# Kernel tuning notes

Hardware: AMD Instinct MI355X
Metric: run time of the kernel (lower is better)

The kernel has to match this reference:

```python
import jax, jax.numpy as jnp
import numpy as np

HEAD_NUM = 16
HIDDEN = 1024
HEAD_DIM = HIDDEN // HEAD_NUM


def setup_inputs() -> dict:
    key = jax.random.key(0)
    ks = jax.random.split(key, 9)
    B, S, D = 1, 4096, HIDDEN
    scale = 1.0 / np.sqrt(D)
    inp = {
        "x": jax.random.normal(ks[0], (B, S, D), jnp.float32),
        "wq": jax.random.normal(ks[1], (D, D), jnp.float32) * scale,
        "bq": jnp.zeros((D,), jnp.float32),
        "wk": jax.random.normal(ks[2], (D, D), jnp.float32) * scale,
        "bk": jnp.zeros((D,), jnp.float32),
        "wv": jax.random.normal(ks[3], (D, D), jnp.float32) * scale,
        "bv": jnp.zeros((D,), jnp.float32),
        "wo": jax.random.normal(ks[4], (D, D), jnp.float32) * scale,
        "bo": jnp.zeros((D,), jnp.float32),
    }
    return inp


def reference(x, wq, bq, wk, bk, wv, bv, wo, bo):
    B, S, D = x.shape
    H, Hd = HEAD_NUM, HEAD_DIM
    # QKV projections (weights stored as [in, out])
    q = (x @ wq + bq).reshape(B, S, H, Hd).transpose(0, 2, 1, 3)  # [B,H,S,Hd]
    k = (x @ wk + bk).reshape(B, S, H, Hd).transpose(0, 2, 1, 3)
    v = (x @ wv + bv).reshape(B, S, H, Hd).transpose(0, 2, 1, 3)
    scores = jnp.einsum("bhqd,bhkd->bhqk", q, k) / jnp.sqrt(jnp.float32(Hd))
    attn = jax.nn.softmax(scores, axis=-1)  # dropout in eval mode = identity
    out = jnp.einsum("bhqk,bhkd->bhqd", attn, v)
    out = out.transpose(0, 2, 1, 3).reshape(B, S, D)
    return out @ wo + bo
```

## Files before the change

kernel.cpp:

```cpp
#include <hip/hip_runtime.h>

#define S_LEN  4096
#define DMODEL 1024
#define NHEAD  16
#define HDIM   64

typedef unsigned short u16;
typedef unsigned int   u32;
typedef __bf16 bf16x8 __attribute__((ext_vector_type(8)));
typedef float  f32x4  __attribute__((ext_vector_type(4)));

static __device__ __forceinline__ u16 f2b(float f) {
    union { __bf16 b; u16 u; } c; c.b = (__bf16)f; return c.u;
}

typedef __attribute__((address_space(3))) u32 lds_u32_t;
typedef __attribute__((address_space(1))) const u32 glb_u32_t;
static __device__ __forceinline__ void gload_lds16(const u16* g, u16* l) {
    __builtin_amdgcn_global_load_lds((glb_u32_t*)g, (lds_u32_t*)l, 16, 0, 0);
}

__global__ __launch_bounds__(256)
void convert_x(const float* __restrict__ x, u16* __restrict__ xb) {
    const int i0 = (blockIdx.x * 256 + threadIdx.x) * 8;
    float4 a = *reinterpret_cast<const float4*>(x + i0);
    float4 b = *reinterpret_cast<const float4*>(x + i0 + 4);
    u16 o[8] = {f2b(a.x), f2b(a.y), f2b(a.z), f2b(a.w),
                f2b(b.x), f2b(b.y), f2b(b.z), f2b(b.w)};
    *reinterpret_cast<uint4*>(xb + i0) = *reinterpret_cast<uint4*>(o);
}

__global__ __launch_bounds__(256)
void transpose_w4(const float* __restrict__ w0, const float* __restrict__ w1,
                  const float* __restrict__ w2, const float* __restrict__ w3,
                  u16* __restrict__ wT) {
    const int z = blockIdx.z;
    const float* w = (z == 0) ? w0 : (z == 1) ? w1 : (z == 2) ? w2 : w3;
    u16* dst0 = wT + (size_t)z * DMODEL * DMODEL;
    const int k0 = blockIdx.x * 64, n0 = blockIdx.y * 64;
    const int t = threadIdx.x;
    __shared__ u16 T[64][72];
    const int kk = t >> 4, nn = (t & 15) * 4;
    #pragma unroll
    for (int i = 0; i < 4; ++i) {
        float4 v = *reinterpret_cast<const float4*>(w + (size_t)(k0 + kk + i * 16) * DMODEL + n0 + nn);
        T[nn + 0][kk + i * 16] = f2b(v.x);
        T[nn + 1][kk + i * 16] = f2b(v.y);
        T[nn + 2][kk + i * 16] = f2b(v.z);
        T[nn + 3][kk + i * 16] = f2b(v.w);
    }
    __syncthreads();
    const int n = t >> 2, kc = (t & 3) * 16;
    uint4 r0 = *reinterpret_cast<const uint4*>(&T[n][kc]);
    uint4 r1 = *reinterpret_cast<const uint4*>(&T[n][kc + 8]);
    u16* dst = dst0 + (size_t)(n0 + n) * DMODEL + k0 + kc;
    *reinterpret_cast<uint4*>(dst)     = r0;
    *reinterpret_cast<uint4*>(dst + 8) = r1;
}

template<int MODE>
__global__ __launch_bounds__(256, 2)
void gemm128(const u16* __restrict__ A, const u16* __restrict__ BT,
             const float* __restrict__ b0, const float* __restrict__ b1,
             const float* __restrict__ b2, void* __restrict__ Cout) {
    const int m0 = blockIdx.x * 128;
    const int ny = blockIdx.y;
    const int tz = (MODE == 0) ? (ny >> 3) : 0;
    const int n0 = (MODE == 0) ? ((ny & 7) * 128) : (ny * 128);
    const int tid = threadIdx.x, lane = tid & 63, w = tid >> 6;
    const int wr = w >> 1, wc = w & 1;
    const int fm = lane & 15, fq = lane >> 4;

    __shared__ u16 As[128][32];
    __shared__ u16 Bs[128][32];

    const u16* Bb = BT + (size_t)tz * DMODEL * DMODEL;

    f32x4 acc[4][4];
    #pragma unroll
    for (int i = 0; i < 4; ++i)
        #pragma unroll
        for (int t = 0; t < 4; ++t) acc[i][t] = f32x4{0.f, 0.f, 0.f, 0.f};

    const int srow = lane >> 2, scol = (lane & 3) * 8;

    for (int k0 = 0; k0 < DMODEL; k0 += 32) {
        #pragma unroll
        for (int r = 0; r < 2; ++r) {
            const int rowA = w * 32 + r * 16;
            gload_lds16(A  + (size_t)(m0 + rowA + srow) * DMODEL + k0 + scol, &As[rowA][0]);
            gload_lds16(Bb + (size_t)(n0 + rowA + srow) * DMODEL + k0 + scol, &Bs[rowA][0]);
        }
        __syncthreads();
        bf16x8 af[4], bf[4];
        #pragma unroll
        for (int i = 0; i < 4; ++i) af[i] = *reinterpret_cast<const bf16x8*>(&As[wr * 64 + i * 16 + fm][fq * 8]);
        #pragma unroll
        for (int t = 0; t < 4; ++t) bf[t] = *reinterpret_cast<const bf16x8*>(&Bs[wc * 64 + t * 16 + fm][fq * 8]);
        #pragma unroll
        for (int i = 0; i < 4; ++i)
            #pragma unroll
            for (int t = 0; t < 4; ++t)
                acc[i][t] = __builtin_amdgcn_mfma_f32_16x16x32_bf16(af[i], bf[t], acc[i][t], 0, 0, 0);
        __syncthreads();
    }

    const float* bp = (MODE == 0) ? ((tz == 0) ? b0 : (tz == 1) ? b1 : b2) : b0;
    #pragma unroll
    for (int t = 0; t < 4; ++t) {
        const int col = n0 + wc * 64 + t * 16 + fm;
        const float bias = bp[col];
        #pragma unroll
        for (int i = 0; i < 4; ++i) {
            #pragma unroll
            for (int r = 0; r < 4; ++r) {
                const int row = m0 + wr * 64 + i * 16 + fq * 4 + r;
                const float v = acc[i][t][r] + bias;
                if (MODE == 0) {
                    const int hh = col >> 6, d = col & 63;
                    ((u16*)Cout)[(size_t)tz * S_LEN * DMODEL + ((size_t)hh * S_LEN + row) * HDIM + d] = f2b(v);
                } else {
                    ((float*)Cout)[(size_t)row * DMODEL + col] = v;
                }
            }
        }
    }
}

__global__ __launch_bounds__(256, 3)
void attn_kernel(const u16* __restrict__ Q, const u16* __restrict__ K,
                 const u16* __restrict__ V, u16* __restrict__ O) {
    const int qt = blockIdx.x, h = blockIdx.y;
    const int tid = threadIdx.x, lane = tid & 63, wid = tid >> 6;
    const int fm = lane & 15, fq = lane >> 4;

    __shared__ alignas(16) u16 Pt[128][68];
    __shared__ alignas(16) u16 Ks[2][64][68];
    __shared__ alignas(16) u16 Vt[2][64][68];

    const u16* Qh = Q + (size_t)h * S_LEN * HDIM;
    const u16* Kh = K + (size_t)h * S_LEN * HDIM;
    const u16* Vh = V + (size_t)h * S_LEN * HDIM;

    const int srow = tid >> 2, sch = (tid & 3) * 16;
    const int kp = tid & 31, vg = (tid >> 5) * 8;

    bf16x8 qf[2][2];
    #pragma unroll
    for (int rb = 0; rb < 2; ++rb) {
        const u16* qsrc = Qh + (size_t)(qt * 128 + wid * 32 + rb * 16 + fm) * HDIM + fq * 8;
        qf[rb][0] = *reinterpret_cast<const bf16x8*>(qsrc);
        qf[rb][1] = *reinterpret_cast<const bf16x8*>(qsrc + 32);
    }

    float rsum[2] = {0.f, 0.f};
    f32x4 oacc[2][4];
    #pragma unroll
    for (int rb = 0; rb < 2; ++rb)
        #pragma unroll
        for (int t = 0; t < 4; ++t) oacc[rb][t] = f32x4{0.f, 0.f, 0.f, 0.f};

    uint4 kr0, kr1, vr0, vr1;
    {
        const u16* ks = Kh + (size_t)srow * HDIM + sch;
        kr0 = *reinterpret_cast<const uint4*>(ks);
        kr1 = *reinterpret_cast<const uint4*>(ks + 8);
        const u16* vs = Vh + (size_t)(2 * kp) * HDIM + vg;
        vr0 = *reinterpret_cast<const uint4*>(vs);
        vr1 = *reinterpret_cast<const uint4*>(vs + HDIM);
    }

    for (int kt = 0; kt < S_LEN / 64; ++kt) {
        const int p = kt & 1;
        *reinterpret_cast<uint4*>(&Ks[p][srow][sch])     = kr0;
        *reinterpret_cast<uint4*>(&Ks[p][srow][sch + 8]) = kr1;
        {
            union { uint4 q; u16 hw[8]; } a, b;
            a.q = vr0; b.q = vr1;
            #pragma unroll
            for (int j = 0; j < 8; ++j) {
                u32 pk = (u32)a.hw[j] | ((u32)b.hw[j] << 16);
                *reinterpret_cast<u32*>(&Vt[p][vg + j][2 * kp]) = pk;
            }
        }
        __syncthreads();

        if (kt + 1 < S_LEN / 64) {
            const u16* ks = Kh + (size_t)((kt + 1) * 64 + srow) * HDIM + sch;
            kr0 = *reinterpret_cast<const uint4*>(ks);
            kr1 = *reinterpret_cast<const uint4*>(ks + 8);
            const u16* vs = Vh + (size_t)((kt + 1) * 64 + 2 * kp) * HDIM + vg;
            vr0 = *reinterpret_cast<const uint4*>(vs);
            vr1 = *reinterpret_cast<const uint4*>(vs + HDIM);
        }

        f32x4 sacc[2][4];
        #pragma unroll
        for (int rb = 0; rb < 2; ++rb)
            #pragma unroll
            for (int mt = 0; mt < 4; ++mt) sacc[rb][mt] = f32x4{0.f, 0.f, 0.f, 0.f};
        #pragma unroll
        for (int kk2 = 0; kk2 < 2; ++kk2) {
            #pragma unroll
            for (int mt = 0; mt < 4; ++mt) {
                bf16x8 kf = *reinterpret_cast<const bf16x8*>(&Ks[p][mt * 16 + fm][kk2 * 32 + fq * 8]);
                #pragma unroll
                for (int rb = 0; rb < 2; ++rb)
                    sacc[rb][mt] = __builtin_amdgcn_mfma_f32_16x16x32_bf16(kf, qf[rb][kk2], sacc[rb][mt], 0, 0, 0);
            }
        }

        #pragma unroll
        for (int rb = 0; rb < 2; ++rb) {
            #pragma unroll
            for (int mt = 0; mt < 4; ++mt) {
                u32 pk[2];
                float e0 = __expf(sacc[rb][mt][0] * 0.125f);
                float e1 = __expf(sacc[rb][mt][1] * 0.125f);
                float e2 = __expf(sacc[rb][mt][2] * 0.125f);
                float e3 = __expf(sacc[rb][mt][3] * 0.125f);
                rsum[rb] += (e0 + e1) + (e2 + e3);
                pk[0] = (u32)f2b(e0) | ((u32)f2b(e1) << 16);
                pk[1] = (u32)f2b(e2) | ((u32)f2b(e3) << 16);
                *reinterpret_cast<uint2*>(&Pt[wid * 32 + rb * 16 + fm][mt * 16 + fq * 4]) =
                    uint2{pk[0], pk[1]};
            }
        }

        #pragma unroll
        for (int kk2 = 0; kk2 < 2; ++kk2) {
            bf16x8 af[2];
            #pragma unroll
            for (int rb = 0; rb < 2; ++rb)
                af[rb] = *reinterpret_cast<const bf16x8*>(&Pt[wid * 32 + rb * 16 + fm][kk2 * 32 + fq * 8]);
            #pragma unroll
            for (int t = 0; t < 4; ++t) {
                bf16x8 bf = *reinterpret_cast<const bf16x8*>(&Vt[p][t * 16 + fm][kk2 * 32 + fq * 8]);
                #pragma unroll
                for (int rb = 0; rb < 2; ++rb)
                    oacc[rb][t] = __builtin_amdgcn_mfma_f32_16x16x32_bf16(af[rb], bf, oacc[rb][t], 0, 0, 0);
            }
        }
    }

    float l[2][4];
    #pragma unroll
    for (int rb = 0; rb < 2; ++rb) {
        float rs = rsum[rb];
        rs += __shfl_xor(rs, 16, 64);
        rs += __shfl_xor(rs, 32, 64);
        #pragma unroll
        for (int r = 0; r < 4; ++r) l[rb][r] = __shfl(rs, fq * 4 + r, 64);
    }

    #pragma unroll
    for (int rb = 0; rb < 2; ++rb)
        #pragma unroll
        for (int t = 0; t < 4; ++t) {
            const int d = t * 16 + fm;
            #pragma unroll
            for (int r = 0; r < 4; ++r) {
                const int row = qt * 128 + wid * 32 + rb * 16 + fq * 4 + r;
                O[(size_t)row * DMODEL + h * HDIM + d] = f2b(oacc[rb][t][r] / l[rb][r]);
            }
        }
}

extern "C" void kernel_launch(void* const* d_in, const int* in_sizes, int n_in,
                              void* d_out, int out_size, void* d_ws, size_t ws_size,
                              hipStream_t stream) {
    const float* x  = (const float*)d_in[0];
    const float* wq = (const float*)d_in[1];
    const float* bq = (const float*)d_in[2];
    const float* wk = (const float*)d_in[3];
    const float* bk = (const float*)d_in[4];
    const float* wv = (const float*)d_in[5];
    const float* bv = (const float*)d_in[6];
    const float* wo = (const float*)d_in[7];
    const float* bo = (const float*)d_in[8];

    u16* ws = (u16*)d_ws;
    const size_t MW  = (size_t)DMODEL * DMODEL;
    const size_t NX  = (size_t)S_LEN * DMODEL;
    const size_t TSZ = (size_t)NHEAD * S_LEN * HDIM;

    u16* xb = ws;
    u16* WT = xb + NX;
    u16* Qb = WT + 4 * MW;
    u16* Ob = Qb + 3 * TSZ;

    hipLaunchKernelGGL(convert_x, dim3(NX / 2048), dim3(256), 0, stream, x, xb);
    hipLaunchKernelGGL(transpose_w4, dim3(16, 16, 4), dim3(256), 0, stream, wq, wk, wv, wo, WT);

    hipLaunchKernelGGL((gemm128<0>), dim3(S_LEN / 128, 24), dim3(256), 0, stream,
                       xb, WT, bq, bk, bv, (void*)Qb);
    hipLaunchKernelGGL(attn_kernel, dim3(S_LEN / 128, NHEAD), dim3(256), 0, stream,
                       Qb, Qb + TSZ, Qb + 2 * TSZ, Ob);
    hipLaunchKernelGGL((gemm128<1>), dim3(S_LEN / 128, 8), dim3(256), 0, stream,
                       Ob, WT + 3 * MW, bo, bo, bo, d_out);
}
```

Measured before the change: 254.9 us.

## Split attention KV range across two blocks, fold softmax scale into Q

Attention now splits the key sequence in two halves along a grid z dimension, writing unnormalized fp32 partial outputs and row sums, and a new combine kernel merges and normalizes them. The intent is to double the block count (512 to 1024) so the GPU is better filled. The softmax scale times log2(e) is folded into the Q projection epilogue so the inner loop can use a raw exp2. LDS double buffering is dropped and occupancy is raised to 4 blocks per CU. The cost is extra fp32 global traffic and an additional kernel launch. The split path only runs if the workspace is large enough, and it still skips max subtraction, which carries an overflow risk.

```diff
diff --git a/kernel.cpp b/kernel.cpp
--- a/kernel.cpp
+++ b/kernel.cpp
@@ -5,6 +5,8 @@
 #define NHEAD  16
 #define HDIM   64
 
+#define QSCALE 0.18033688011112042f
+
 typedef unsigned short u16;
 typedef unsigned int   u32;
 typedef __bf16 bf16x8 __attribute__((ext_vector_type(8)));
@@ -12,6 +14,14 @@
 
 static __device__ __forceinline__ u16 f2b(float f) {
     union { __bf16 b; u16 u; } c; c.b = (__bf16)f; return c.u;
+}
+
+static __device__ __forceinline__ float fexp2(float x) {
+#if __has_builtin(__builtin_amdgcn_exp2f)
+    return __builtin_amdgcn_exp2f(x);
+#else
+    return __expf(x * 0.6931471805599453f);
+#endif
 }
 
 typedef __attribute__((address_space(3))) u32 lds_u32_t;
@@ -106,6 +116,7 @@
     }
 
     const float* bp = (MODE == 0) ? ((tz == 0) ? b0 : (tz == 1) ? b1 : b2) : b0;
+    const float scl = (MODE == 0 && tz == 0) ? QSCALE : 1.0f;
     #pragma unroll
     for (int t = 0; t < 4; ++t) {
         const int col = n0 + wc * 64 + t * 16 + fm;
@@ -115,7 +126,7 @@
             #pragma unroll
             for (int r = 0; r < 4; ++r) {
                 const int row = m0 + wr * 64 + i * 16 + fq * 4 + r;
-                const float v = acc[i][t][r] + bias;
+                const float v = (acc[i][t][r] + bias) * scl;
                 if (MODE == 0) {
                     const int hh = col >> 6, d = col & 63;
                     ((u16*)Cout)[(size_t)tz * S_LEN * DMODEL + ((size_t)hh * S_LEN + row) * HDIM + d] = f2b(v);
@@ -127,16 +138,19 @@
     }
 }
 
-__global__ __launch_bounds__(256, 3)
+template<int NSPLIT>
+__global__ __launch_bounds__(256, 4)
 void attn_kernel(const u16* __restrict__ Q, const u16* __restrict__ K,
-                 const u16* __restrict__ V, u16* __restrict__ O) {
+                 const u16* __restrict__ V, void* __restrict__ Optr,
+                 float* __restrict__ Lp) {
     const int qt = blockIdx.x, h = blockIdx.y;
+    const int sp = (NSPLIT == 2) ? blockIdx.z : 0;
     const int tid = threadIdx.x, lane = tid & 63, wid = tid >> 6;
     const int fm = lane & 15, fq = lane >> 4;
 
     __shared__ alignas(16) u16 Pt[128][68];
-    __shared__ alignas(16) u16 Ks[2][64][68];
-    __shared__ alignas(16) u16 Vt[2][64][68];
+    __shared__ alignas(16) u16 Ks[64][68];
+    __shared__ alignas(16) u16 Vt[64][68];
 
     const u16* Qh = Q + (size_t)h * S_LEN * HDIM;
     const u16* Kh = K + (size_t)h * S_LEN * HDIM;
@@ -160,32 +174,36 @@
         #pragma unroll
         for (int t = 0; t < 4; ++t) oacc[rb][t] = f32x4{0.f, 0.f, 0.f, 0.f};
 
+    const int NT  = S_LEN / 64 / NSPLIT;
+    const int kt0 = sp * NT;
+
     uint4 kr0, kr1, vr0, vr1;
     {
-        const u16* ks = Kh + (size_t)srow * HDIM + sch;
+        const u16* ks = Kh + (size_t)(kt0 * 64 + srow) * HDIM + sch;
         kr0 = *reinterpret_cast<const uint4*>(ks);
         kr1 = *reinterpret_cast<const uint4*>(ks + 8);
-        const u16* vs = Vh + (size_t)(2 * kp) * HDIM + vg;
+        const u16* vs = Vh + (size_t)(kt0 * 64 + 2 * kp) * HDIM + vg;
         vr0 = *reinterpret_cast<const uint4*>(vs);
         vr1 = *reinterpret_cast<const uint4*>(vs + HDIM);
     }
 
-    for (int kt = 0; kt < S_LEN / 64; ++kt) {
-        const int p = kt & 1;
-        *reinterpret_cast<uint4*>(&Ks[p][srow][sch])     = kr0;
-        *reinterpret_cast<uint4*>(&Ks[p][srow][sch + 8]) = kr1;
+    for (int it = 0; it < NT; ++it) {
+        const int kt = kt0 + it;
+        __syncthreads();
+        *reinterpret_cast<uint4*>(&Ks[srow][sch])     = kr0;
+        *reinterpret_cast<uint4*>(&Ks[srow][sch + 8]) = kr1;
         {
             union { uint4 q; u16 hw[8]; } a, b;
             a.q = vr0; b.q = vr1;
             #pragma unroll
             for (int j = 0; j < 8; ++j) {
                 u32 pk = (u32)a.hw[j] | ((u32)b.hw[j] << 16);
-                *reinterpret_cast<u32*>(&Vt[p][vg + j][2 * kp]) = pk;
+                *reinterpret_cast<u32*>(&Vt[vg + j][2 * kp]) = pk;
             }
         }
         __syncthreads();
 
-        if (kt + 1 < S_LEN / 64) {
+        if (it + 1 < NT) {
             const u16* ks = Kh + (size_t)((kt + 1) * 64 + srow) * HDIM + sch;
             kr0 = *reinterpret_cast<const uint4*>(ks);
             kr1 = *reinterpret_cast<const uint4*>(ks + 8);
@@ -203,7 +221,7 @@
         for (int kk2 = 0; kk2 < 2; ++kk2) {
             #pragma unroll
             for (int mt = 0; mt < 4; ++mt) {
-                bf16x8 kf = *reinterpret_cast<const bf16x8*>(&Ks[p][mt * 16 + fm][kk2 * 32 + fq * 8]);
+                bf16x8 kf = *reinterpret_cast<const bf16x8*>(&Ks[mt * 16 + fm][kk2 * 32 + fq * 8]);
                 #pragma unroll
                 for (int rb = 0; rb < 2; ++rb)
                     sacc[rb][mt] = __builtin_amdgcn_mfma_f32_16x16x32_bf16(kf, qf[rb][kk2], sacc[rb][mt], 0, 0, 0);
@@ -215,10 +233,10 @@
             #pragma unroll
             for (int mt = 0; mt < 4; ++mt) {
                 u32 pk[2];
-                float e0 = __expf(sacc[rb][mt][0] * 0.125f);
-                float e1 = __expf(sacc[rb][mt][1] * 0.125f);
-                float e2 = __expf(sacc[rb][mt][2] * 0.125f);
-                float e3 = __expf(sacc[rb][mt][3] * 0.125f);
+                float e0 = fexp2(sacc[rb][mt][0]);
+                float e1 = fexp2(sacc[rb][mt][1]);
+                float e2 = fexp2(sacc[rb][mt][2]);
+                float e3 = fexp2(sacc[rb][mt][3]);
                 rsum[rb] += (e0 + e1) + (e2 + e3);
                 pk[0] = (u32)f2b(e0) | ((u32)f2b(e1) << 16);
                 pk[1] = (u32)f2b(e2) | ((u32)f2b(e3) << 16);
@@ -235,7 +253,7 @@
                 af[rb] = *reinterpret_cast<const bf16x8*>(&Pt[wid * 32 + rb * 16 + fm][kk2 * 32 + fq * 8]);
             #pragma unroll
             for (int t = 0; t < 4; ++t) {
-                bf16x8 bf = *reinterpret_cast<const bf16x8*>(&Vt[p][t * 16 + fm][kk2 * 32 + fq * 8]);
+                bf16x8 bf = *reinterpret_cast<const bf16x8*>(&Vt[t * 16 + fm][kk2 * 32 + fq * 8]);
                 #pragma unroll
                 for (int rb = 0; rb < 2; ++rb)
                     oacc[rb][t] = __builtin_amdgcn_mfma_f32_16x16x32_bf16(af[rb], bf, oacc[rb][t], 0, 0, 0);
@@ -243,27 +261,65 @@
         }
     }
 
-    float l[2][4];
-    #pragma unroll
-    for (int rb = 0; rb < 2; ++rb) {
-        float rs = rsum[rb];
-        rs += __shfl_xor(rs, 16, 64);
-        rs += __shfl_xor(rs, 32, 64);
-        #pragma unroll
-        for (int r = 0; r < 4; ++r) l[rb][r] = __shfl(rs, fq * 4 + r, 64);
-    }
-
-    #pragma unroll
-    for (int rb = 0; rb < 2; ++rb)
-        #pragma unroll
-        for (int t = 0; t < 4; ++t) {
-            const int d = t * 16 + fm;
-            #pragma unroll
-            for (int r = 0; r < 4; ++r) {
-                const int row = qt * 128 + wid * 32 + rb * 16 + fq * 4 + r;
-                O[(size_t)row * DMODEL + h * HDIM + d] = f2b(oacc[rb][t][r] / l[rb][r]);
-            }
-        }
+    if (NSPLIT == 2) {
+        float* Op = (float*)Optr + (size_t)sp * S_LEN * DMODEL;
+        #pragma unroll
+        for (int rb = 0; rb < 2; ++rb) {
+            float rs = rsum[rb];
+            rs += __shfl_xor(rs, 16, 64);
+            rs += __shfl_xor(rs, 32, 64);
+            if (fq == 0)
+                Lp[(size_t)sp * NHEAD * S_LEN + (size_t)h * S_LEN +
+                   qt * 128 + wid * 32 + rb * 16 + fm] = rs;
+            #pragma unroll
+            for (int t = 0; t < 4; ++t) {
+                const int d = t * 16 + fm;
+                #pragma unroll
+                for (int r = 0; r < 4; ++r) {
+                    const int row = qt * 128 + wid * 32 + rb * 16 + fq * 4 + r;
+                    Op[(size_t)row * DMODEL + h * HDIM + d] = oacc[rb][t][r];
+                }
+            }
+        }
+    } else {
+        float l[2][4];
+        #pragma unroll
+        for (int rb = 0; rb < 2; ++rb) {
+            float rs = rsum[rb];
+            rs += __shfl_xor(rs, 16, 64);
+            rs += __shfl_xor(rs, 32, 64);
+            #pragma unroll
+            for (int r = 0; r < 4; ++r) l[rb][r] = __shfl(rs, fq * 4 + r, 64);
+        }
+        u16* O = (u16*)Optr;
+        #pragma unroll
+        for (int rb = 0; rb < 2; ++rb)
+            #pragma unroll
+            for (int t = 0; t < 4; ++t) {
+                const int d = t * 16 + fm;
+                #pragma unroll
+                for (int r = 0; r < 4; ++r) {
+                    const int row = qt * 128 + wid * 32 + rb * 16 + fq * 4 + r;
+                    O[(size_t)row * DMODEL + h * HDIM + d] = f2b(oacc[rb][t][r] / l[rb][r]);
+                }
+            }
+    }
+}
+
+__global__ __launch_bounds__(256)
+void combine_o(const float* __restrict__ Op, const float* __restrict__ Lp,
+               u16* __restrict__ Ob) {
+    const size_t i = ((size_t)blockIdx.x * 256 + threadIdx.x) * 4;
+    const int row = (int)(i >> 10), col = (int)(i & 1023);
+    const int h = col >> 6;
+    float4 a = *reinterpret_cast<const float4*>(Op + i);
+    float4 b = *reinterpret_cast<const float4*>(Op + (size_t)S_LEN * DMODEL + i);
+    const float l = Lp[(size_t)h * S_LEN + row] +
+                    Lp[(size_t)NHEAD * S_LEN + (size_t)h * S_LEN + row];
+    const float inv = 1.0f / l;
+    u16 o[4] = {f2b((a.x + b.x) * inv), f2b((a.y + b.y) * inv),
+                f2b((a.z + b.z) * inv), f2b((a.w + b.w) * inv)};
+    *reinterpret_cast<uint2*>(Ob + i) = *reinterpret_cast<uint2*>(o);
 }
 
 extern "C" void kernel_launch(void* const* d_in, const int* in_sizes, int n_in,
@@ -288,14 +344,27 @@
     u16* WT = xb + NX;
     u16* Qb = WT + 4 * MW;
     u16* Ob = Qb + 3 * TSZ;
+    float* Op = (float*)(Ob + NX);
+    float* Lp = Op + (size_t)2 * NX;
+    const size_t need = (size_t)((char*)(Lp + (size_t)2 * NHEAD * S_LEN) - (char*)d_ws);
+    const bool split = (ws_size >= need);
 
     hipLaunchKernelGGL(convert_x, dim3(NX / 2048), dim3(256), 0, stream, x, xb);
     hipLaunchKernelGGL(transpose_w4, dim3(16, 16, 4), dim3(256), 0, stream, wq, wk, wv, wo, WT);
 
     hipLaunchKernelGGL((gemm128<0>), dim3(S_LEN / 128, 24), dim3(256), 0, stream,
                        xb, WT, bq, bk, bv, (void*)Qb);
-    hipLaunchKernelGGL(attn_kernel, dim3(S_LEN / 128, NHEAD), dim3(256), 0, stream,
-                       Qb, Qb + TSZ, Qb + 2 * TSZ, Ob);
+
+    if (split) {
+        hipLaunchKernelGGL((attn_kernel<2>), dim3(S_LEN / 128, NHEAD, 2), dim3(256), 0, stream,
+                           Qb, Qb + TSZ, Qb + 2 * TSZ, (void*)Op, Lp);
+        hipLaunchKernelGGL(combine_o, dim3((S_LEN * DMODEL / 4) / 256), dim3(256), 0, stream,
+                           Op, Lp, Ob);
+    } else {
+        hipLaunchKernelGGL((attn_kernel<1>), dim3(S_LEN / 128, NHEAD, 1), dim3(256), 0, stream,
+                           Qb, Qb + TSZ, Qb + 2 * TSZ, (void*)Ob, (float*)nullptr);
+    }
+
     hipLaunchKernelGGL((gemm128<1>), dim3(S_LEN / 128, 8), dim3(256), 0, stream,
                        Ob, WT + 3 * MW, bo, bo, bo, d_out);
 }
```

Result: no change. 250.7 us (-1.6%).
